# Kernel tuning notes

Measured on AMD Instinct MI355X. Metric: run time of the kernel, lower is better.

Reference implementation:

```python
import jax, jax.numpy as jnp
import numpy as np

B, N_O, N_Q = 2, 512, 512
POS_DIM, LATENT, HEADS, HEAD_DIM, OUT_DIM = 3, 256, 8, 32, 128
HD = HEADS * HEAD_DIM  # == LATENT here


def _lin(key, fan_in, fan_out):
    return jax.random.normal(key, (fan_in, fan_out), jnp.float32) / np.sqrt(fan_in)


def setup_inputs() -> dict:
    key = jax.random.key(0)
    ks = jax.random.split(key, 12)
    return {
        'h_obs': jax.random.normal(ks[0], (B, N_O, LATENT), jnp.float32),
        'pos_obs': jax.random.uniform(ks[1], (B, N_O, POS_DIM), jnp.float32),
        'pos_query': jax.random.uniform(ks[2], (B, N_Q, POS_DIM), jnp.float32),
        'fw1': _lin(ks[3], LATENT, LATENT), 'fb1': jnp.zeros((LATENT,), jnp.float32),
        'fw2': _lin(ks[4], LATENT, HD), 'fb2': jnp.zeros((HD,), jnp.float32),
        'log_sigma': jnp.zeros((HEADS,), jnp.float32),
        'kw1': _lin(ks[5], POS_DIM * 3, LATENT), 'kb1': jnp.zeros((LATENT,), jnp.float32),
        'kw2': _lin(ks[6], LATENT, HEADS), 'kb2': jnp.zeros((HEADS,), jnp.float32),
        'ow': _lin(ks[7], HD, OUT_DIM), 'ob': jnp.zeros((OUT_DIM,), jnp.float32),
        'vw': _lin(ks[8], HD, OUT_DIM), 'vb': jnp.zeros((OUT_DIM,), jnp.float32),
    }


def reference(h_obs, pos_obs, pos_query, fw1, fb1, fw2, fb2, log_sigma,
              kw1, kb1, kw2, kb2, ow, ob, vw, vb):
    Bv, No, _ = h_obs.shape
    Nq = pos_query.shape[1]
    # feature net -> values [B, H, N_o, D]
    v = jax.nn.relu(h_obs @ fw1 + fb1) @ fw2 + fb2
    v = v.reshape(Bv, No, HEADS, HEAD_DIM).transpose(0, 2, 1, 3)
    # pairwise relative positions [B, Nq, No, P]
    pos_q = pos_query[:, :, None, :]
    pos_o = pos_obs[:, None, :, :]
    rel = pos_q - pos_o
    dist2 = jnp.sum(rel ** 2, axis=-1)  # [B, Nq, No]
    sigma = jnp.exp(log_sigma)[None, :, None, None]
    rbf = jnp.exp(-dist2[:, None] / (sigma ** 2 + 1e-6))  # [B, H, Nq, No]
    # kernel MLP on concatenated pairwise positions [B, Nq, No, 3P] -> [B, H, Nq, No]
    ki = jnp.concatenate([
        jnp.broadcast_to(pos_q, (Bv, Nq, No, POS_DIM)),
        jnp.broadcast_to(pos_o, (Bv, Nq, No, POS_DIM)),
        rel], axis=-1)
    delta = (jax.nn.relu(ki @ kw1 + kb1) @ kw2 + kb2).transpose(0, 3, 1, 2)
    logits = jnp.log(rbf + 1e-8) + delta
    weights = jax.nn.softmax(logits, axis=-1)  # [B, H, Nq, No]
    # weighted mean over observations
    v_mean = jnp.einsum('bhqo,bhod->bhqd', weights, v)  # [B, H, Nq, D]
    h_query = v_mean.transpose(0, 2, 1, 3).reshape(Bv, Nq, HD)
    # weighted variance: sum_o w * (v_o - v_mean)^2
    residual = v[:, :, None, :, :] - v_mean[:, :, :, None, :]  # [B, H, Nq, No, D]
    var = jnp.sum(weights[..., None] * residual ** 2, axis=3)  # [B, H, Nq, D]
    var = var.transpose(0, 2, 1, 3).reshape(Bv, Nq, HD)
    mean = h_query @ ow + ob
    var_out = jax.nn.softplus(var @ vw + vb)
    return (mean, var_out)
```

## Files before the change

kernel.cpp:

```cpp
#include <hip/hip_runtime.h>
#include <math.h>

#define NB 2
#define NO 512
#define NQ 512
#define OUT_DIM 128
#define LPAD 520

typedef __attribute__((ext_vector_type(8))) short short8;
typedef __attribute__((ext_vector_type(4))) float f32x4;
typedef float v2f __attribute__((ext_vector_type(2)));

__device__ __forceinline__ float softplus_f(float x) {
  return x > 0.0f ? x + log1pf(expf(-x)) : log1pf(expf(x));
}
__device__ __forceinline__ unsigned short bf16_rne(float f) {
  unsigned u = __float_as_uint(f);
  unsigned r = u + 0x7FFFu + ((u >> 16) & 1u);
  return (unsigned short)(r >> 16);
}
__device__ __forceinline__ float bf16_to_f32(unsigned short h) {
  return __uint_as_float(((unsigned)h) << 16);
}
__device__ __forceinline__ unsigned pack_bf2(float x, float y) {
  unsigned ux = __float_as_uint(x);
  unsigned uy = __float_as_uint(y);
  ux = ux + 0x7FFFu + ((ux >> 16) & 1u);
  uy = uy + 0x7FFFu + ((uy >> 16) & 1u);
  return (ux >> 16) | (uy & 0xFFFF0000u);
}
__device__ __forceinline__ v2f unpk_bf2(unsigned u) {
  v2f r; r.x = __uint_as_float(u << 16); r.y = __uint_as_float(u & 0xFFFF0000u);
  return r;
}
__device__ __forceinline__ v2f splat2(float x) { v2f r; r.x = x; r.y = x; return r; }
__device__ __forceinline__ v2f fma2(v2f a, v2f b, v2f c) { return __builtin_elementwise_fma(a, b, c); }
__device__ __forceinline__ v2f max2(v2f a, v2f b) { return __builtin_elementwise_max(a, b); }

__global__ __launch_bounds__(1024) void prep_kernel(
    const float* __restrict__ h_obs, const float* __restrict__ fw1,
    const float* __restrict__ fb1, const float* __restrict__ fw2,
    const float* __restrict__ fb2, const float* __restrict__ pos_obs,
    const float* __restrict__ kw1, unsigned short* __restrict__ V_bf,
    unsigned short* __restrict__ AO_bf)
{
  if (blockIdx.x < 256) {
    __shared__ float s_red[4][4][256];
    __shared__ float s_hid[4][256];
    const int n  = threadIdx.x & 255;
    const int ks = threadIdx.x >> 8;
    const int r0 = blockIdx.x * 4;
    const int k0 = ks * 64;
    float a0 = 0.f, a1 = 0.f, a2 = 0.f, a3 = 0.f;
    #pragma unroll 8
    for (int kk = 0; kk < 64; ++kk) {
      int k = k0 + kk;
      float w = fw1[k * 256 + n];
      a0 = fmaf(h_obs[(r0 + 0) * 256 + k], w, a0);
      a1 = fmaf(h_obs[(r0 + 1) * 256 + k], w, a1);
      a2 = fmaf(h_obs[(r0 + 2) * 256 + k], w, a2);
      a3 = fmaf(h_obs[(r0 + 3) * 256 + k], w, a3);
    }
    s_red[ks][0][n] = a0; s_red[ks][1][n] = a1;
    s_red[ks][2][n] = a2; s_red[ks][3][n] = a3;
    __syncthreads();
    if (ks == 0) {
      float bb = fb1[n];
      #pragma unroll
      for (int r = 0; r < 4; ++r) {
        float v = s_red[0][r][n] + s_red[1][r][n] + s_red[2][r][n] + s_red[3][r][n] + bb;
        s_hid[r][n] = fmaxf(v, 0.f);
      }
    }
    __syncthreads();
    float c0 = 0.f, c1 = 0.f, c2 = 0.f, c3 = 0.f;
    #pragma unroll 8
    for (int kk = 0; kk < 64; ++kk) {
      int k = k0 + kk;
      float w = fw2[k * 256 + n];
      c0 = fmaf(s_hid[0][k], w, c0);
      c1 = fmaf(s_hid[1][k], w, c1);
      c2 = fmaf(s_hid[2][k], w, c2);
      c3 = fmaf(s_hid[3][k], w, c3);
    }
    __syncthreads();
    s_red[ks][0][n] = c0; s_red[ks][1][n] = c1;
    s_red[ks][2][n] = c2; s_red[ks][3][n] = c3;
    __syncthreads();
    if (ks == 0) {
      float bb = fb2[n];
      #pragma unroll
      for (int r = 0; r < 4; ++r) {
        float v = s_red[0][r][n] + s_red[1][r][n] + s_red[2][r][n] + s_red[3][r][n] + bb;
        V_bf[(size_t)(r0 + r) * 256 + n] = bf16_rne(v);
      }
    }
  } else {
    const int i  = blockIdx.x - 256;
    const int b  = i >> 7;
    const int og = i & 127;
    const int ol = threadIdx.x >> 8;
    const int j  = threadIdx.x & 255;
    const int o  = og * 4 + ol;
    float c0 = kw1[3 * 256 + j] - kw1[6 * 256 + j];
    float c1 = kw1[4 * 256 + j] - kw1[7 * 256 + j];
    float c2 = kw1[5 * 256 + j] - kw1[8 * 256 + j];
    const float* p = pos_obs + ((size_t)(b * NO + o)) * 3;
    AO_bf[(size_t)(b * NO + o) * 256 + j] =
        bf16_rne(fmaf(p[0], c0, fmaf(p[1], c1, p[2] * c2)));
  }
}

__global__ __launch_bounds__(512, 4) void attn_fused(
    const unsigned short* __restrict__ V_bf,
    const unsigned short* __restrict__ AO_bf,
    const float* __restrict__ kw1,
    const float* __restrict__ kb1,
    const float* __restrict__ kw2,
    const float* __restrict__ kb2,
    const float* __restrict__ log_sigma,
    const float* __restrict__ pos_obs,
    const float* __restrict__ pos_query,
    const float* __restrict__ ow, const float* __restrict__ obias,
    const float* __restrict__ vw, const float* __restrict__ vbias,
    float* __restrict__ out)
{
  __shared__ float s_logits[2][8 * LPAD];
  __shared__ __align__(16) char poolA[18432];
  __shared__ __align__(16) char poolB[4096];
  __shared__ float s_sum[2][8];

  short8* Bhi    = (short8*)poolA;
  short8* Blo    = (short8*)(poolA + 8192);
  float*  s_redA = (float*)poolA;
  float*  s_pred = (float*)poolA;
  float*  s_aq   = (float*)poolB;
  float*  s_hv   = (float*)poolB;

  const int t   = threadIdx.x;
  const int bq0 = blockIdx.x * 2;
  const int b   = bq0 >> 9;

  float pqx[2], pqy[2], pqz[2];
  #pragma unroll
  for (int q = 0; q < 2; ++q) {
    pqx[q] = pos_query[(bq0 + q) * 3 + 0];
    pqy[q] = pos_query[(bq0 + q) * 3 + 1];
    pqz[q] = pos_query[(bq0 + q) * 3 + 2];
  }
  {
    const int q = t >> 8, j = t & 255;
    float c0 = kw1[0 * 256 + j] + kw1[6 * 256 + j];
    float c1 = kw1[1 * 256 + j] + kw1[7 * 256 + j];
    float c2 = kw1[2 * 256 + j] + kw1[8 * 256 + j];
    s_aq[q * 256 + j] =
        fmaf(pqx[q], c0, fmaf(pqy[q], c1, fmaf(pqz[q], c2, kb1[j])));
  }
  {
    const int o = t;
    const float* p = pos_obs + (size_t)(b * NO + o) * 3;
    float px = p[0], py = p[1], pz = p[2];
    float d2q[2];
    #pragma unroll
    for (int q = 0; q < 2; ++q) {
      float r0 = pqx[q] - px, r1 = pqy[q] - py, r2 = pqz[q] - pz;
      d2q[q] = r0 * r0 + r1 * r1 + r2 * r2;
    }
    #pragma unroll
    for (int h = 0; h < 8; ++h) {
      float sg  = expf(log_sigma[h]);
      float inv = 1.0f / (sg * sg + 1e-6f);
      float kbv = kb2[h];
      s_logits[0][h * LPAD + o] = logf(expf(-d2q[0] * inv) + 1e-8f) + kbv;
      s_logits[1][h * LPAD + o] = logf(expf(-d2q[1] * inv) + 1e-8f) + kbv;
    }
  }
  {
    const int kstep = t >> 6, lane = t & 63;
    const int nh = lane & 15;
    const int kb_ = kstep * 32 + ((lane >> 4) & 3) * 8;
    short8 hi8, lo8;
    #pragma unroll
    for (int i = 0; i < 8; ++i) {
      float v = (nh < 8) ? kw2[(kb_ + i) * 8 + nh] : 0.f;
      unsigned short h = bf16_rne(v);
      hi8[i] = (short)h;
      lo8[i] = (short)bf16_rne(v - bf16_to_f32(h));
    }
    Bhi[kstep * 64 + lane] = hi8;
    Blo[kstep * 64 + lane] = lo8;
  }
  __syncthreads();

  {
    const int wave = t >> 6, lane = t & 63;
    const int quad = lane >> 4, mrow = lane & 15;
    const int tb   = wave * 4;
    f32x4 C[2][4];
    #pragma unroll
    for (int q = 0; q < 2; ++q)
      #pragma unroll
      for (int jt = 0; jt < 4; ++jt) C[q][jt] = (f32x4){0.f, 0.f, 0.f, 0.f};

    for (int kstep = 0; kstep < 8; ++kstep) {
      const int koff = kstep * 32 + quad * 8;
      const v2f* aqp0 = (const v2f*)(s_aq + koff);
      const v2f* aqp1 = (const v2f*)(s_aq + 256 + koff);
      v2f aq0[4], aq1[4];
      #pragma unroll
      for (int i = 0; i < 4; ++i) { aq0[i] = aqp0[i]; aq1[i] = aqp1[i]; }
      short8 bhi = Bhi[kstep * 64 + lane];
      short8 blo = Blo[kstep * 64 + lane];
      #pragma unroll
      for (int jt = 0; jt < 4; ++jt) {
        const int o = (tb + jt) * 16 + mrow;
        int4 u = *(const int4*)(AO_bf + ((size_t)(b * NO + o) << 8) + koff);
        v2f ao[4];
        ao[0] = unpk_bf2((unsigned)u.x); ao[1] = unpk_bf2((unsigned)u.y);
        ao[2] = unpk_bf2((unsigned)u.z); ao[3] = unpk_bf2((unsigned)u.w);
        v2f z = splat2(0.f);
        int4 af0, af1;
        {
          v2f h0 = max2(aq0[0] + ao[0], z), h1 = max2(aq0[1] + ao[1], z);
          v2f h2 = max2(aq0[2] + ao[2], z), h3 = max2(aq0[3] + ao[3], z);
          af0.x = (int)pack_bf2(h0.x, h0.y); af0.y = (int)pack_bf2(h1.x, h1.y);
          af0.z = (int)pack_bf2(h2.x, h2.y); af0.w = (int)pack_bf2(h3.x, h3.y);
        }
        {
          v2f h0 = max2(aq1[0] + ao[0], z), h1 = max2(aq1[1] + ao[1], z);
          v2f h2 = max2(aq1[2] + ao[2], z), h3 = max2(aq1[3] + ao[3], z);
          af1.x = (int)pack_bf2(h0.x, h0.y); af1.y = (int)pack_bf2(h1.x, h1.y);
          af1.z = (int)pack_bf2(h2.x, h2.y); af1.w = (int)pack_bf2(h3.x, h3.y);
        }
        short8 a0 = __builtin_bit_cast(short8, af0);
        short8 a1 = __builtin_bit_cast(short8, af1);
        C[0][jt] = __builtin_amdgcn_mfma_f32_16x16x32_bf16(a0, bhi, C[0][jt], 0, 0, 0);
        C[0][jt] = __builtin_amdgcn_mfma_f32_16x16x32_bf16(a0, blo, C[0][jt], 0, 0, 0);
        C[1][jt] = __builtin_amdgcn_mfma_f32_16x16x32_bf16(a1, bhi, C[1][jt], 0, 0, 0);
        C[1][jt] = __builtin_amdgcn_mfma_f32_16x16x32_bf16(a1, blo, C[1][jt], 0, 0, 0);
      }
    }
    const int h = lane & 15;
    if (h < 8) {
      #pragma unroll
      for (int q = 0; q < 2; ++q)
        #pragma unroll
        for (int jt = 0; jt < 4; ++jt) {
          const int ob = (tb + jt) * 16 + quad * 4;
          #pragma unroll
          for (int r = 0; r < 4; ++r)
            s_logits[q][h * LPAD + ob + r] += C[q][jt][r];
        }
    }
  }
  __syncthreads();

  {
    const int wave = t >> 6, lane = t & 63;
    #pragma unroll
    for (int cc = 0; cc < 2; ++cc) {
      const int c = wave * 2 + cc;
      const int q = c >> 3, h = c & 7;
      float* pl = &s_logits[q][h * LPAD];
      float l[8];
      float m = -1e30f;
      #pragma unroll
      for (int k = 0; k < 8; ++k) {
        l[k] = pl[k * 64 + lane];
        m = fmaxf(m, l[k]);
      }
      #pragma unroll
      for (int off = 32; off >= 1; off >>= 1) m = fmaxf(m, __shfl_xor(m, off, 64));
      float s = 0.f;
      #pragma unroll
      for (int k = 0; k < 8; ++k) {
        float p = expf(l[k] - m);
        pl[k * 64 + lane] = p;
        s += p;
      }
      #pragma unroll
      for (int off = 32; off >= 1; off >>= 1) s += __shfl_xor(s, off, 64);
      if (lane == 0) s_sum[q][h] = s;
    }
  }
  __syncthreads();

  float q1p[8];
  {
    const int s  = t >> 6;
    const int r  = t & 63;
    const int h  = r >> 3, dg = r & 7;
    const unsigned short* vb_ = V_bf + ((size_t)(b * NO) << 8) + h * 32 + dg * 4;
    const float* P0 = &s_logits[0][h * LPAD];
    const float* P1 = &s_logits[1][h * LPAD];
    v2f s1a0 = splat2(0.f), s1b0 = splat2(0.f), s2a0 = splat2(0.f), s2b0 = splat2(0.f);
    v2f s1a1 = splat2(0.f), s1b1 = splat2(0.f), s2a1 = splat2(0.f), s2b1 = splat2(0.f);
    const int o0 = s * 64;
    #pragma unroll 4
    for (int oi = 0; oi < 64; ++oi) {
      const int o = o0 + oi;
      uint2 vv = *(const uint2*)(vb_ + ((size_t)o << 8));
      v2f va  = unpk_bf2(vv.x);
      v2f vb2 = unpk_bf2(vv.y);
      v2f p0 = splat2(P0[o]), p1 = splat2(P1[o]);
      s1a0 = fma2(p0, va, s1a0);  s1b0 = fma2(p0, vb2, s1b0);
      v2f t0a = p0 * va, t0b = p0 * vb2;
      s2a0 = fma2(t0a, va, s2a0); s2b0 = fma2(t0b, vb2, s2b0);
      s1a1 = fma2(p1, va, s1a1);  s1b1 = fma2(p1, vb2, s1b1);
      v2f t1a = p1 * va, t1b = p1 * vb2;
      s2a1 = fma2(t1a, va, s2a1); s2b1 = fma2(t1b, vb2, s2b1);
    }
    float* row = s_redA + t * 9;
    row[0] = s1a0.x; row[1] = s1a0.y; row[2] = s1b0.x; row[3] = s1b0.y;
    row[4] = s2a0.x; row[5] = s2a0.y; row[6] = s2b0.x; row[7] = s2b0.y;
    q1p[0] = s1a1.x; q1p[1] = s1a1.y; q1p[2] = s1b1.x; q1p[3] = s1b1.y;
    q1p[4] = s2a1.x; q1p[5] = s2a1.y; q1p[6] = s2b1.x; q1p[7] = s2b1.y;
  }
  __syncthreads();
  if (t < 256) {
    const int hd = t, h = hd >> 5, d = hd & 31, dg = d >> 2, c = d & 3;
    float S1 = 0.f, S2 = 0.f;
    #pragma unroll
    for (int s = 0; s < 8; ++s) {
      const float* row = s_redA + (size_t)(s * 64 + h * 8 + dg) * 9;
      S1 += row[c]; S2 += row[4 + c];
    }
    float inv = 1.0f / s_sum[0][h];
    float m1 = S1 * inv;
    float va = fmaxf(S2 * inv - m1 * m1, 0.f);
    s_hv[0 * 256 + hd] = m1;
    s_hv[1 * 256 + hd] = va;
  }
  __syncthreads();
  {
    float* row = s_redA + t * 9;
    #pragma unroll
    for (int i = 0; i < 8; ++i) row[i] = q1p[i];
  }
  __syncthreads();
  if (t < 256) {
    const int hd = t, h = hd >> 5, d = hd & 31, dg = d >> 2, c = d & 3;
    float S1 = 0.f, S2 = 0.f;
    #pragma unroll
    for (int s = 0; s < 8; ++s) {
      const float* row = s_redA + (size_t)(s * 64 + h * 8 + dg) * 9;
      S1 += row[c]; S2 += row[4 + c];
    }
    float inv = 1.0f / s_sum[1][h];
    float m1 = S1 * inv;
    float va = fmaxf(S2 * inv - m1 * m1, 0.f);
    s_hv[2 * 256 + hd] = m1;
    s_hv[3 * 256 + hd] = va;
  }
  __syncthreads();

  {
    const int ks = t >> 8, mode = (t >> 7) & 1, n = t & 127;
    const float* W  = mode ? vw : ow;
    const float* X0 = s_hv + mode * 256;
    const float* X1 = s_hv + (2 + mode) * 256;
    float a0 = 0.f, a1 = 0.f;
    const int k0 = ks * 128;
    #pragma unroll 4
    for (int k = k0; k < k0 + 128; k += 4) {
      float4 x0 = *(const float4*)&X0[k];
      float4 x1 = *(const float4*)&X1[k];
      float w0 = W[(k + 0) * 128 + n];
      float w1 = W[(k + 1) * 128 + n];
      float w2 = W[(k + 2) * 128 + n];
      float w3 = W[(k + 3) * 128 + n];
      a0 = fmaf(x0.x, w0, a0); a1 = fmaf(x1.x, w0, a1);
      a0 = fmaf(x0.y, w1, a0); a1 = fmaf(x1.y, w1, a1);
      a0 = fmaf(x0.z, w2, a0); a1 = fmaf(x1.z, w2, a1);
      a0 = fmaf(x0.w, w3, a0); a1 = fmaf(x1.w, w3, a1);
    }
    __syncthreads();
    s_pred[((ks * 2 + mode) * 2 + 0) * 128 + n] = a0;
    s_pred[((ks * 2 + mode) * 2 + 1) * 128 + n] = a1;
  }
  __syncthreads();
  {
    const int q = t >> 8, mode = (t >> 7) & 1, n = t & 127;
    float v = s_pred[((0 * 2 + mode) * 2 + q) * 128 + n]
            + s_pred[((1 * 2 + mode) * 2 + q) * 128 + n]
            + (mode ? vbias[n] : obias[n]);
    if (mode) v = softplus_f(v);
    out[(size_t)mode * (NB * NQ * OUT_DIM) + (size_t)(bq0 + q) * OUT_DIM + n] = v;
  }
}

extern "C" void kernel_launch(void* const* d_in, const int* in_sizes, int n_in,
                              void* d_out, int out_size, void* d_ws, size_t ws_size,
                              hipStream_t stream)
{
  const float* h_obs     = (const float*)d_in[0];
  const float* pos_obs   = (const float*)d_in[1];
  const float* pos_query = (const float*)d_in[2];
  const float* fw1       = (const float*)d_in[3];
  const float* fb1       = (const float*)d_in[4];
  const float* fw2       = (const float*)d_in[5];
  const float* fb2       = (const float*)d_in[6];
  const float* log_sigma = (const float*)d_in[7];
  const float* kw1       = (const float*)d_in[8];
  const float* kb1       = (const float*)d_in[9];
  const float* kw2       = (const float*)d_in[10];
  const float* kb2       = (const float*)d_in[11];
  const float* ow        = (const float*)d_in[12];
  const float* ob        = (const float*)d_in[13];
  const float* vw        = (const float*)d_in[14];
  const float* vb        = (const float*)d_in[15];

  float* out = (float*)d_out;
  unsigned short* ws = (unsigned short*)d_ws;

  unsigned short* V_bf  = ws;
  unsigned short* AO_bf = ws + 262144;

  prep_kernel<<<512, 1024, 0, stream>>>(h_obs, fw1, fb1, fw2, fb2,
                                        pos_obs, kw1, V_bf, AO_bf);
  attn_fused<<<NB * NQ / 2, 512, 0, stream>>>(V_bf, AO_bf, kw1, kb1, kw2, kb2,
                                              log_sigma, pos_obs, pos_query,
                                              ow, ob, vw, vb, out);
}
```

Measured before the change: 150.9 us.

## Use single fp16 MFMA for kernel MLP and shuffle-reduce weighted moments

Replaces the split hi/lo bf16 MFMA pair with one fp16 MFMA per tile, halving matrix work, and converts the hidden activations with packed round-to-zero fp16 conversion. The weighted mean/variance pass is remapped so each wave handles one head, with rotated observation indexing and wave butterfly shuffles replacing the shared-memory partial-sum reductions and several barriers. It also switches to fast __expf/__logf intrinsics, shrinks the logits row padding, and removes a redundant barrier. The cost is lower precision in the delta logits (fp16 with no hi/lo compensation) and in the transcendentals.

```diff
diff --git a/kernel.cpp b/kernel.cpp
--- a/kernel.cpp
+++ b/kernel.cpp
@@ -5,9 +5,10 @@
 #define NO 512
 #define NQ 512
 #define OUT_DIM 128
-#define LPAD 520
+#define LPAD 514
 
 typedef __attribute__((ext_vector_type(8))) short short8;
+typedef __attribute__((ext_vector_type(8))) _Float16 half8;
 typedef __attribute__((ext_vector_type(4))) float f32x4;
 typedef float v2f __attribute__((ext_vector_type(2)));
 
@@ -19,16 +20,6 @@
   unsigned r = u + 0x7FFFu + ((u >> 16) & 1u);
   return (unsigned short)(r >> 16);
 }
-__device__ __forceinline__ float bf16_to_f32(unsigned short h) {
-  return __uint_as_float(((unsigned)h) << 16);
-}
-__device__ __forceinline__ unsigned pack_bf2(float x, float y) {
-  unsigned ux = __float_as_uint(x);
-  unsigned uy = __float_as_uint(y);
-  ux = ux + 0x7FFFu + ((ux >> 16) & 1u);
-  uy = uy + 0x7FFFu + ((uy >> 16) & 1u);
-  return (ux >> 16) | (uy & 0xFFFF0000u);
-}
 __device__ __forceinline__ v2f unpk_bf2(unsigned u) {
   v2f r; r.x = __uint_as_float(u << 16); r.y = __uint_as_float(u & 0xFFFF0000u);
   return r;
@@ -36,6 +27,17 @@
 __device__ __forceinline__ v2f splat2(float x) { v2f r; r.x = x; r.y = x; return r; }
 __device__ __forceinline__ v2f fma2(v2f a, v2f b, v2f c) { return __builtin_elementwise_fma(a, b, c); }
 __device__ __forceinline__ v2f max2(v2f a, v2f b) { return __builtin_elementwise_max(a, b); }
+__device__ __forceinline__ int cvt2h(float x, float y) {
+  return __builtin_bit_cast(int, __builtin_amdgcn_cvt_pkrtz(x, y));
+}
+__device__ __forceinline__ v2f bfly_s(v2f x) {
+  #pragma unroll
+  for (int off = 8; off <= 32; off <<= 1) {
+    x.x += __shfl_xor(x.x, off, 64);
+    x.y += __shfl_xor(x.y, off, 64);
+  }
+  return x;
+}
 
 __global__ __launch_bounds__(1024) void prep_kernel(
     const float* __restrict__ h_obs, const float* __restrict__ fw1,
@@ -126,16 +128,13 @@
     float* __restrict__ out)
 {
   __shared__ float s_logits[2][8 * LPAD];
-  __shared__ __align__(16) char poolA[18432];
-  __shared__ __align__(16) char poolB[4096];
+  __shared__ half8 s_Bh[512];
+  __shared__ __align__(16) float s_pool[2048];
   __shared__ float s_sum[2][8];
 
-  short8* Bhi    = (short8*)poolA;
-  short8* Blo    = (short8*)(poolA + 8192);
-  float*  s_redA = (float*)poolA;
-  float*  s_pred = (float*)poolA;
-  float*  s_aq   = (float*)poolB;
-  float*  s_hv   = (float*)poolB;
+  float* s_aq   = s_pool;
+  float* s_hv   = s_pool;
+  float* s_pred = s_pool + 1024;
 
   const int t   = threadIdx.x;
   const int bq0 = blockIdx.x * 2;
@@ -168,27 +167,24 @@
     }
     #pragma unroll
     for (int h = 0; h < 8; ++h) {
-      float sg  = expf(log_sigma[h]);
+      float sg  = __expf(log_sigma[h]);
       float inv = 1.0f / (sg * sg + 1e-6f);
       float kbv = kb2[h];
-      s_logits[0][h * LPAD + o] = logf(expf(-d2q[0] * inv) + 1e-8f) + kbv;
-      s_logits[1][h * LPAD + o] = logf(expf(-d2q[1] * inv) + 1e-8f) + kbv;
+      s_logits[0][h * LPAD + o] = __logf(__expf(-d2q[0] * inv) + 1e-8f) + kbv;
+      s_logits[1][h * LPAD + o] = __logf(__expf(-d2q[1] * inv) + 1e-8f) + kbv;
     }
   }
   {
     const int kstep = t >> 6, lane = t & 63;
     const int nh = lane & 15;
     const int kb_ = kstep * 32 + ((lane >> 4) & 3) * 8;
-    short8 hi8, lo8;
+    half8 b8;
     #pragma unroll
     for (int i = 0; i < 8; ++i) {
       float v = (nh < 8) ? kw2[(kb_ + i) * 8 + nh] : 0.f;
-      unsigned short h = bf16_rne(v);
-      hi8[i] = (short)h;
-      lo8[i] = (short)bf16_rne(v - bf16_to_f32(h));
-    }
-    Bhi[kstep * 64 + lane] = hi8;
-    Blo[kstep * 64 + lane] = lo8;
+      b8[i] = (_Float16)v;
+    }
+    s_Bh[kstep * 64 + lane] = b8;
   }
   __syncthreads();
 
@@ -209,47 +205,43 @@
       v2f aq0[4], aq1[4];
       #pragma unroll
       for (int i = 0; i < 4; ++i) { aq0[i] = aqp0[i]; aq1[i] = aqp1[i]; }
-      short8 bhi = Bhi[kstep * 64 + lane];
-      short8 blo = Blo[kstep * 64 + lane];
+      half8 bh = s_Bh[kstep * 64 + lane];
       #pragma unroll
       for (int jt = 0; jt < 4; ++jt) {
         const int o = (tb + jt) * 16 + mrow;
-        int4 u = *(const int4*)(AO_bf + ((size_t)(b * NO + o) << 8) + koff);
-        v2f ao[4];
-        ao[0] = unpk_bf2((unsigned)u.x); ao[1] = unpk_bf2((unsigned)u.y);
-        ao[2] = unpk_bf2((unsigned)u.z); ao[3] = unpk_bf2((unsigned)u.w);
+        int4 u = *(const int4*)(AO_bf + ((b * NO + o) << 8) + koff);
+        v2f ao0 = unpk_bf2((unsigned)u.x), ao1 = unpk_bf2((unsigned)u.y);
+        v2f ao2 = unpk_bf2((unsigned)u.z), ao3 = unpk_bf2((unsigned)u.w);
         v2f z = splat2(0.f);
         int4 af0, af1;
         {
-          v2f h0 = max2(aq0[0] + ao[0], z), h1 = max2(aq0[1] + ao[1], z);
-          v2f h2 = max2(aq0[2] + ao[2], z), h3 = max2(aq0[3] + ao[3], z);
-          af0.x = (int)pack_bf2(h0.x, h0.y); af0.y = (int)pack_bf2(h1.x, h1.y);
-          af0.z = (int)pack_bf2(h2.x, h2.y); af0.w = (int)pack_bf2(h3.x, h3.y);
+          v2f h0 = max2(aq0[0] + ao0, z), h1 = max2(aq0[1] + ao1, z);
+          v2f h2 = max2(aq0[2] + ao2, z), h3 = max2(aq0[3] + ao3, z);
+          af0.x = cvt2h(h0.x, h0.y); af0.y = cvt2h(h1.x, h1.y);
+          af0.z = cvt2h(h2.x, h2.y); af0.w = cvt2h(h3.x, h3.y);
         }
         {
-          v2f h0 = max2(aq1[0] + ao[0], z), h1 = max2(aq1[1] + ao[1], z);
-          v2f h2 = max2(aq1[2] + ao[2], z), h3 = max2(aq1[3] + ao[3], z);
-          af1.x = (int)pack_bf2(h0.x, h0.y); af1.y = (int)pack_bf2(h1.x, h1.y);
-          af1.z = (int)pack_bf2(h2.x, h2.y); af1.w = (int)pack_bf2(h3.x, h3.y);
+          v2f h0 = max2(aq1[0] + ao0, z), h1 = max2(aq1[1] + ao1, z);
+          v2f h2 = max2(aq1[2] + ao2, z), h3 = max2(aq1[3] + ao3, z);
+          af1.x = cvt2h(h0.x, h0.y); af1.y = cvt2h(h1.x, h1.y);
+          af1.z = cvt2h(h2.x, h2.y); af1.w = cvt2h(h3.x, h3.y);
         }
-        short8 a0 = __builtin_bit_cast(short8, af0);
-        short8 a1 = __builtin_bit_cast(short8, af1);
-        C[0][jt] = __builtin_amdgcn_mfma_f32_16x16x32_bf16(a0, bhi, C[0][jt], 0, 0, 0);
-        C[0][jt] = __builtin_amdgcn_mfma_f32_16x16x32_bf16(a0, blo, C[0][jt], 0, 0, 0);
-        C[1][jt] = __builtin_amdgcn_mfma_f32_16x16x32_bf16(a1, bhi, C[1][jt], 0, 0, 0);
-        C[1][jt] = __builtin_amdgcn_mfma_f32_16x16x32_bf16(a1, blo, C[1][jt], 0, 0, 0);
-      }
-    }
-    const int h = lane & 15;
-    if (h < 8) {
+        half8 a0 = __builtin_bit_cast(half8, af0);
+        half8 a1 = __builtin_bit_cast(half8, af1);
+        C[0][jt] = __builtin_amdgcn_mfma_f32_16x16x32_f16(a0, bh, C[0][jt], 0, 0, 0);
+        C[1][jt] = __builtin_amdgcn_mfma_f32_16x16x32_f16(a1, bh, C[1][jt], 0, 0, 0);
+      }
+    }
+    const int hh = lane & 15;
+    if (hh < 8) {
       #pragma unroll
       for (int q = 0; q < 2; ++q)
         #pragma unroll
         for (int jt = 0; jt < 4; ++jt) {
-          const int ob = (tb + jt) * 16 + quad * 4;
+          const int ob2 = (tb + jt) * 16 + quad * 4;
           #pragma unroll
           for (int r = 0; r < 4; ++r)
-            s_logits[q][h * LPAD + ob + r] += C[q][jt][r];
+            s_logits[q][hh * LPAD + ob2 + r] += C[q][jt][r];
         }
     }
   }
@@ -274,7 +266,7 @@
       float s = 0.f;
       #pragma unroll
       for (int k = 0; k < 8; ++k) {
-        float p = expf(l[k] - m);
+        float p = __expf(l[k] - m);
         pl[k * 64 + lane] = p;
         s += p;
       }
@@ -285,72 +277,62 @@
   }
   __syncthreads();
 
-  float q1p[8];
-  {
-    const int s  = t >> 6;
-    const int r  = t & 63;
-    const int h  = r >> 3, dg = r & 7;
-    const unsigned short* vb_ = V_bf + ((size_t)(b * NO) << 8) + h * 32 + dg * 4;
+  {
+    const int h  = t >> 6;
+    const int l  = t & 63;
+    const int s5 = l >> 3;
+    const int dg = l & 7;
+    const unsigned short* vb_ = V_bf + ((b * NO) << 8) + h * 32 + dg * 4;
     const float* P0 = &s_logits[0][h * LPAD];
     const float* P1 = &s_logits[1][h * LPAD];
-    v2f s1a0 = splat2(0.f), s1b0 = splat2(0.f), s2a0 = splat2(0.f), s2b0 = splat2(0.f);
-    v2f s1a1 = splat2(0.f), s1b1 = splat2(0.f), s2a1 = splat2(0.f), s2b1 = splat2(0.f);
-    const int o0 = s * 64;
+    v2f A0 = splat2(0.f), B0 = A0, C0 = A0, D0 = A0;
+    v2f A1 = A0, B1 = A0, C1 = A0, D1 = A0;
+    const int ob = s5 * 64, rot = s5 * 8;
     #pragma unroll 4
-    for (int oi = 0; oi < 64; ++oi) {
-      const int o = o0 + oi;
-      uint2 vv = *(const uint2*)(vb_ + ((size_t)o << 8));
-      v2f va  = unpk_bf2(vv.x);
-      v2f vb2 = unpk_bf2(vv.y);
-      v2f p0 = splat2(P0[o]), p1 = splat2(P1[o]);
-      s1a0 = fma2(p0, va, s1a0);  s1b0 = fma2(p0, vb2, s1b0);
-      v2f t0a = p0 * va, t0b = p0 * vb2;
-      s2a0 = fma2(t0a, va, s2a0); s2b0 = fma2(t0b, vb2, s2b0);
-      s1a1 = fma2(p1, va, s1a1);  s1b1 = fma2(p1, vb2, s1b1);
-      v2f t1a = p1 * va, t1b = p1 * vb2;
-      s2a1 = fma2(t1a, va, s2a1); s2b1 = fma2(t1b, vb2, s2b1);
-    }
-    float* row = s_redA + t * 9;
-    row[0] = s1a0.x; row[1] = s1a0.y; row[2] = s1b0.x; row[3] = s1b0.y;
-    row[4] = s2a0.x; row[5] = s2a0.y; row[6] = s2b0.x; row[7] = s2b0.y;
-    q1p[0] = s1a1.x; q1p[1] = s1a1.y; q1p[2] = s1b1.x; q1p[3] = s1b1.y;
-    q1p[4] = s2a1.x; q1p[5] = s2a1.y; q1p[6] = s2b1.x; q1p[7] = s2b1.y;
-  }
-  __syncthreads();
-  if (t < 256) {
-    const int hd = t, h = hd >> 5, d = hd & 31, dg = d >> 2, c = d & 3;
-    float S1 = 0.f, S2 = 0.f;
-    #pragma unroll
-    for (int s = 0; s < 8; ++s) {
-      const float* row = s_redA + (size_t)(s * 64 + h * 8 + dg) * 9;
-      S1 += row[c]; S2 += row[4 + c];
-    }
-    float inv = 1.0f / s_sum[0][h];
-    float m1 = S1 * inv;
-    float va = fmaxf(S2 * inv - m1 * m1, 0.f);
-    s_hv[0 * 256 + hd] = m1;
-    s_hv[1 * 256 + hd] = va;
-  }
-  __syncthreads();
-  {
-    float* row = s_redA + t * 9;
-    #pragma unroll
-    for (int i = 0; i < 8; ++i) row[i] = q1p[i];
-  }
-  __syncthreads();
-  if (t < 256) {
-    const int hd = t, h = hd >> 5, d = hd & 31, dg = d >> 2, c = d & 3;
-    float S1 = 0.f, S2 = 0.f;
-    #pragma unroll
-    for (int s = 0; s < 8; ++s) {
-      const float* row = s_redA + (size_t)(s * 64 + h * 8 + dg) * 9;
-      S1 += row[c]; S2 += row[4 + c];
-    }
-    float inv = 1.0f / s_sum[1][h];
-    float m1 = S1 * inv;
-    float va = fmaxf(S2 * inv - m1 * m1, 0.f);
-    s_hv[2 * 256 + hd] = m1;
-    s_hv[3 * 256 + hd] = va;
+    for (int oi = 0; oi < 64; oi += 2) {
+      const int oo = ob + ((oi + rot) & 63);
+      v2f p0 = *(const v2f*)(P0 + oo);
+      v2f p1 = *(const v2f*)(P1 + oo);
+      uint2 v0 = *(const uint2*)(vb_ + (oo << 8));
+      uint2 v1 = *(const uint2*)(vb_ + ((oo + 1) << 8));
+      v2f va0 = unpk_bf2(v0.x), vb0 = unpk_bf2(v0.y);
+      v2f va1 = unpk_bf2(v1.x), vb1 = unpk_bf2(v1.y);
+      v2f t0, t1;
+      v2f p00 = splat2(p0.x), p10 = splat2(p1.x);
+      A0 = fma2(p00, va0, A0); B0 = fma2(p00, vb0, B0);
+      t0 = p00 * va0; C0 = fma2(t0, va0, C0);
+      t1 = p00 * vb0; D0 = fma2(t1, vb0, D0);
+      A1 = fma2(p10, va0, A1); B1 = fma2(p10, vb0, B1);
+      t0 = p10 * va0; C1 = fma2(t0, va0, C1);
+      t1 = p10 * vb0; D1 = fma2(t1, vb0, D1);
+      v2f p01 = splat2(p0.y), p11 = splat2(p1.y);
+      A0 = fma2(p01, va1, A0); B0 = fma2(p01, vb1, B0);
+      t0 = p01 * va1; C0 = fma2(t0, va1, C0);
+      t1 = p01 * vb1; D0 = fma2(t1, vb1, D0);
+      A1 = fma2(p11, va1, A1); B1 = fma2(p11, vb1, B1);
+      t0 = p11 * va1; C1 = fma2(t0, va1, C1);
+      t1 = p11 * vb1; D1 = fma2(t1, vb1, D1);
+    }
+    A0 = bfly_s(A0); B0 = bfly_s(B0); C0 = bfly_s(C0); D0 = bfly_s(D0);
+    A1 = bfly_s(A1); B1 = bfly_s(B1); C1 = bfly_s(C1); D1 = bfly_s(D1);
+    if (s5 < 4) {
+      const int q = s5 >> 1, kind = s5 & 1;
+      v2f S1a = q ? A1 : A0, S1b = q ? B1 : B0;
+      v2f S2a = q ? C1 : C0, S2b = q ? D1 : D0;
+      float inv = 1.0f / s_sum[q][h];
+      float m0 = S1a.x * inv, m1 = S1a.y * inv;
+      float m2 = S1b.x * inv, m3 = S1b.y * inv;
+      float4 w;
+      if (kind == 0) {
+        w = (float4){m0, m1, m2, m3};
+      } else {
+        w = (float4){fmaxf(S2a.x * inv - m0 * m0, 0.f),
+                     fmaxf(S2a.y * inv - m1 * m1, 0.f),
+                     fmaxf(S2b.x * inv - m2 * m2, 0.f),
+                     fmaxf(S2b.y * inv - m3 * m3, 0.f)};
+      }
+      *(float4*)(s_hv + (q * 2 + kind) * 256 + h * 32 + dg * 4) = w;
+    }
   }
   __syncthreads();
 
@@ -374,7 +356,6 @@
       a0 = fmaf(x0.z, w2, a0); a1 = fmaf(x1.z, w2, a1);
       a0 = fmaf(x0.w, w3, a0); a1 = fmaf(x1.w, w3, a1);
     }
-    __syncthreads();
     s_pred[((ks * 2 + mode) * 2 + 0) * 128 + n] = a0;
     s_pred[((ks * 2 + mode) * 2 + 1) * 128 + n] = a1;
   }
```

Result: faster. 139.5 us (-7.6%).
